# Performance work log

Hardware: AMD Instinct MI355X
Metric: run time of the kernel (lower is better)

## Reference

```python
import jax, jax.numpy as jnp
import numpy as np

B, S, F, H, D = 32, 512, 32, 8, 300   # batch, seq, n_features, hidden_dim, n_dim_model
FH = min(D, F)                        # flattened GRN hidden = min(n_dim_model, n_features)


def _p(key, shape, scale=0.05):
    return (jax.random.normal(key, shape) * scale).astype(jnp.float32)


def setup_inputs() -> dict:
    key = jax.random.key(0)
    ks = jax.random.split(key, 16)
    return {
        "x": jax.random.normal(ks[0], (B, S, F), dtype=jnp.float32),
        "pre_w": _p(ks[1], (F, H)), "pre_b": _p(ks[2], (F, H)),
        "sg_fc1_w": _p(ks[3], (F, H, H)), "sg_fc1_b": _p(ks[4], (F, H)),
        "sg_fc2_w": _p(ks[5], (F, H, D)), "sg_fc2_b": _p(ks[6], (F, D)),
        "sg_gate_w": _p(ks[7], (F, D, 2 * D)), "sg_gate_b": _p(ks[8], (F, 2 * D)),
        "sg_ln_g": jnp.ones((F, D), jnp.float32), "sg_ln_b": jnp.zeros((F, D), jnp.float32),
        "fl_fc1_w": _p(ks[9], (F * H, FH)), "fl_fc1_b": _p(ks[10], (FH,)),
        "fl_fc2_w": _p(ks[11], (FH, F)), "fl_fc2_b": _p(ks[12], (F,)),
        "fl_gate_w": _p(ks[13], (F, 2 * F)), "fl_gate_b": _p(ks[14], (2 * F,)),
        "fl_ln_g": jnp.ones((F,), jnp.float32), "fl_ln_b": jnp.zeros((F,), jnp.float32),
    }


def _interp_last(x, out_dim):
    # torch F.interpolate(mode='linear', align_corners=True) along the last axis
    in_dim = x.shape[-1]
    pos = jnp.arange(out_dim) * ((in_dim - 1) / (out_dim - 1))
    lo = jnp.floor(pos).astype(jnp.int32)
    hi = jnp.minimum(lo + 1, in_dim - 1)
    w = (pos - lo.astype(pos.dtype)).astype(x.dtype)
    return x[..., lo] * (1 - w) + x[..., hi] * w


def _layer_norm(x, g, b, eps=1e-5):
    m = jnp.mean(x, axis=-1, keepdims=True)
    v = jnp.var(x, axis=-1, keepdims=True)
    return (x - m) * jax.lax.rsqrt(v + eps) * g + b


def _forward(x, pre_w, pre_b, sg_fc1_w, sg_fc1_b, sg_fc2_w, sg_fc2_b,
             sg_gate_w, sg_gate_b, sg_ln_g, sg_ln_b,
             fl_fc1_w, fl_fc1_b, fl_fc2_w, fl_fc2_b, fl_gate_w, fl_gate_b,
             fl_ln_g, fl_ln_b):
    # per-feature prescaler: Linear(1, H) for each of F features, batched
    pre = x[..., None] * pre_w + pre_b                                   # [B,S,F,H]

    # per-feature GRN (H -> H -> D), batched over the feature axis f
    h = jax.nn.elu(jnp.einsum('bsfh,fhk->bsfk', pre, sg_fc1_w) + sg_fc1_b)
    h = jnp.einsum('bsfk,fkd->bsfd', h, sg_fc2_w) + sg_fc2_b             # [B,S,F,D]
    g = jnp.einsum('bsfd,fdp->bsfp', h, sg_gate_w) + sg_gate_b           # [B,S,F,2D]
    glu = g[..., :D] * jax.nn.sigmoid(g[..., D:])
    residual = _interp_last(pre, D)                                      # H -> D interpolate projection
    outputs = _layer_norm(glu + residual, sg_ln_g, sg_ln_b)              # [B,S,F,D]

    # flattened GRN on concatenated prescaler outputs (F*H -> FH -> F)
    flat = pre.reshape(pre.shape[0], pre.shape[1], F * H)                # matches torch.cat order
    fh = jax.nn.elu(flat @ fl_fc1_w + fl_fc1_b)
    fh = fh @ fl_fc2_w + fl_fc2_b                                        # [B,S,F]
    fg = fh @ fl_gate_w + fl_gate_b                                      # [B,S,2F]
    fglu = fg[..., :F] * jax.nn.sigmoid(fg[..., F:])
    wlogits = _layer_norm(fglu + _interp_last(flat, F), fl_ln_g, fl_ln_b)
    w = jax.nn.softmax(wlogits, axis=-1)                                 # [B,S,F]

    out = jnp.einsum('bsfd,bsf->bsd', outputs, w)                        # softmax-weighted sum over features
    return out, w[..., None, :]                                          # weights unsqueezed at dim -2


def reference(x, pre_w, pre_b, sg_fc1_w, sg_fc1_b, sg_fc2_w, sg_fc2_b,
              sg_gate_w, sg_gate_b, sg_ln_g, sg_ln_b,
              fl_fc1_w, fl_fc1_b, fl_fc2_w, fl_fc2_b, fl_gate_w, fl_gate_b,
              fl_ln_g, fl_ln_b):
    return _forward(x, pre_w, pre_b, sg_fc1_w, sg_fc1_b, sg_fc2_w, sg_fc2_b,
                    sg_gate_w, sg_gate_b, sg_ln_g, sg_ln_b,
                    fl_fc1_w, fl_fc1_b, fl_fc2_w, fl_fc2_b, fl_gate_w, fl_gate_b,
                    fl_ln_g, fl_ln_b)
```

## Files before the change

kernel.cpp:

```cpp
#include <hip/hip_runtime.h>
#include <hip/hip_bf16.h>

#define NB 32
#define NS 512
#define NF 32
#define NH 8
#define ND 300
#define NTOK (NB*NS)
#define TPW 8
#define WPB 4
#define TPB (TPW*WPB)

using bf16 = __hip_bfloat16;
typedef float v2f __attribute__((ext_vector_type(2)));

__device__ __forceinline__ float rcpf_(float x){ return __builtin_amdgcn_rcpf(x); }
__device__ __forceinline__ float rsqf_(float x){ return __builtin_amdgcn_rsqf(x); }
__device__ __forceinline__ float sigm(float x){ return rcpf_(1.0f + __expf(-x)); }
__device__ __forceinline__ float eluf(float x){ return x > 0.0f ? x : __expf(x) - 1.0f; }

__device__ __forceinline__ v2f fma2(v2f a, v2f b, v2f c){
    return __builtin_elementwise_fma(a, b, c);
}
__device__ __forceinline__ v2f fma2s(float s, v2f b, v2f c){
    return __builtin_elementwise_fma((v2f){s, s}, b, c);
}

template<int BF16>
__device__ __forceinline__ float ldf(const void* p, size_t i){
    if (BF16) return __bfloat162float(((const bf16*)p)[i]);
    return ((const float*)p)[i];
}
template<int BF16>
__device__ __forceinline__ void stf(void* p, size_t i, float v){
    if (BF16) ((bf16*)p)[i] = __float2bfloat16(v);
    else      ((float*)p)[i] = v;
}

__device__ __forceinline__ bool is_bf16(const void* ones){
    return *(const unsigned*)ones == 0x3F803F80u;
}

__device__ __forceinline__ v2f unpk(unsigned u){
    return (v2f){ __int_as_float((int)(u << 16)),
                  __int_as_float((int)(u & 0xFFFF0000u)) };
}
__device__ __forceinline__ unsigned pack_bf(float a, float b){
    bf16 ha = __float2bfloat16(a), hb = __float2bfloat16(b);
    return (unsigned)*(unsigned short*)&ha | ((unsigned)*(unsigned short*)&hb << 16);
}

template<int CTRL>
__device__ __forceinline__ float dppadd(float v){
    return v + __int_as_float(__builtin_amdgcn_update_dpp(
        0, __float_as_int(v), CTRL, 0xF, 0xF, true));
}
template<int CTRL>
__device__ __forceinline__ float dppmax(float v){
    return fmaxf(v, __int_as_float(__builtin_amdgcn_update_dpp(
        __float_as_int(v), __float_as_int(v), CTRL, 0xF, 0xF, false)));
}
__device__ __forceinline__ float rlane(float v, int l){
    return __int_as_float(__builtin_amdgcn_readlane(__float_as_int(v), l));
}
__device__ __forceinline__ float wsum64(float v){
    v = dppadd<0x111>(v); v = dppadd<0x112>(v); v = dppadd<0x114>(v); v = dppadd<0x118>(v);
    v = dppadd<0x142>(v); v = dppadd<0x143>(v);
    return rlane(v, 63);
}
__device__ __forceinline__ float rsum32(float v){
    v = dppadd<0x111>(v); v = dppadd<0x112>(v); v = dppadd<0x114>(v); v = dppadd<0x118>(v);
    return rlane(v, 15) + rlane(v, 31);
}
__device__ __forceinline__ float rmax32(float v){
    v = dppmax<0x111>(v); v = dppmax<0x112>(v); v = dppmax<0x114>(v); v = dppmax<0x118>(v);
    return fmaxf(rlane(v, 15), rlane(v, 31));
}

template<int BF16>
__device__ void precompute_body(const void* __restrict__ W2, const void* __restrict__ b2,
                                const void* __restrict__ Wg, const void* __restrict__ bg,
                                const void* __restrict__ sg_g, const void* __restrict__ sg_b,
                                unsigned* __restrict__ Crow,
                                float (*part)[64][18], float (*w2s)[2400], float (*b2s)[300])
{
    const int tid = threadIdx.x;
    const int l = tid & 63;
    const int q = tid >> 6;
    const int fd = blockIdx.x * 64 + l;
    const int f = fd / 300;
    const int d = fd % 300;

    const int fLo = (blockIdx.x * 64) / 300;
    const int fHi = (blockIdx.x * 64 + 63) / 300;

    for (int ff = 0; ff <= fHi - fLo; ++ff) {
        for (int idx = tid; idx < 2400; idx += 256)
            w2s[ff][idx] = ldf<BF16>(W2, (size_t)(fLo + ff) * 2400 + idx);
        for (int idx = tid; idx < 300; idx += 256)
            b2s[ff][idx] = ldf<BF16>(b2, (size_t)(fLo + ff) * 300 + idx);
    }
    __syncthreads();

    const float* myW2 = w2s[f - fLo];
    const float* myB2 = b2s[f - fLo];
    const size_t WgA = (size_t)f * 180000 + d;

    float accA[8] = {0,0,0,0,0,0,0,0};
    float accB[8] = {0,0,0,0,0,0,0,0};
    float bA = 0.f, bB = 0.f;
    for (int m = q * 75; m < q * 75 + 75; ++m) {
        float wa = ldf<BF16>(Wg, WgA + (size_t)m * 600);
        float wb = ldf<BF16>(Wg, WgA + (size_t)m * 600 + 300);
        #pragma unroll
        for (int k = 0; k < 8; ++k) {
            float w2v = myW2[k * 300 + m];
            accA[k] += w2v * wa;
            accB[k] += w2v * wb;
        }
        bA += myB2[m] * wa;
        bB += myB2[m] * wb;
    }
    #pragma unroll
    for (int k = 0; k < 8; ++k) { part[q][l][k] = accA[k]; part[q][l][8 + k] = accB[k]; }
    part[q][l][16] = bA;
    part[q][l][17] = bB;
    __syncthreads();

    unsigned* row = Crow + (size_t)fd * 12;
    for (int v = q; v < 12; v += 4) {
        if (v < 8) {
            float sA = part[0][l][v] + part[1][l][v] + part[2][l][v] + part[3][l][v];
            float sB = part[0][l][8+v] + part[1][l][8+v] + part[2][l][8+v] + part[3][l][8+v];
            row[v] = pack_bf(sA, sB);
        } else if (v == 8) {
            float s = part[0][l][16] + part[1][l][16] + part[2][l][16] + part[3][l][16];
            float bc = s + ldf<BF16>(bg, (size_t)f * 600 + d);
            row[8] = __float_as_uint(bc);
        } else if (v == 9) {
            float s = part[0][l][17] + part[1][l][17] + part[2][l][17] + part[3][l][17];
            float bc = s + ldf<BF16>(bg, (size_t)f * 600 + d + 300);
            row[9] = __float_as_uint(bc);
        } else if (v == 10) {
            row[10] = __float_as_uint(ldf<BF16>(sg_g, (size_t)f * 300 + d));
        } else {
            row[11] = __float_as_uint(ldf<BF16>(sg_b, (size_t)f * 300 + d));
        }
    }
}

__global__ void precompute_kernel(const void* __restrict__ W2, const void* __restrict__ b2,
                                  const void* __restrict__ Wg, const void* __restrict__ bg,
                                  const void* __restrict__ sg_g, const void* __restrict__ sg_b,
                                  unsigned* __restrict__ Crow)
{
    __shared__ float part[4][64][18];
    __shared__ float w2s[2][2400];
    __shared__ float b2s[2][300];
    if (is_bf16(sg_g))
        precompute_body<1>(W2, b2, Wg, bg, sg_g, sg_b, Crow, part, w2s, b2s);
    else
        precompute_body<0>(W2, b2, Wg, bg, sg_g, sg_b, Crow, part, w2s, b2s);
}

template<int BF16>
__device__ void vsn_body(const void* __restrict__ x,
                         const void* __restrict__ pre_w, const void* __restrict__ pre_b,
                         const void* __restrict__ W1,    const void* __restrict__ b1,
                         const void* __restrict__ fl1w,  const void* __restrict__ fl1b,
                         const void* __restrict__ fl2w,  const void* __restrict__ fl2b,
                         const void* __restrict__ flgw,  const void* __restrict__ flgb,
                         const void* __restrict__ flng,  const void* __restrict__ flnb,
                         const unsigned* __restrict__ Crow,
                         void* __restrict__ d_out, float* preS_, float* hS_)
{
    void* outMain = d_out;
    void* outW    = (char*)d_out + (size_t)NTOK * ND * (BF16 ? 2 : 4);

    const int tid  = threadIdx.x;
    const int wave = tid >> 6;
    const int lane = tid & 63;
    const int tokBase = blockIdx.x * TPB + wave * TPW;

    float* myPre = preS_ + wave * (TPW * 256);
    float* myH   = hS_   + wave * (TPW * 256);

    {
        float pw[4], pb[4];
        #pragma unroll
        for (int q = 0; q < 4; ++q) {
            pw[q] = ldf<BF16>(pre_w, 4 * lane + q);
            pb[q] = ldf<BF16>(pre_b, 4 * lane + q);
        }
        const int fidx = lane >> 1;
        #pragma unroll
        for (int t = 0; t < TPW; ++t) {
            float xv = ldf<BF16>(x, (size_t)(tokBase + t) * NF + fidx);
            float4 v;
            v.x = xv * pw[0] + pb[0];
            v.y = xv * pw[1] + pb[1];
            v.z = xv * pw[2] + pb[2];
            v.w = xv * pw[3] + pb[3];
            *(float4*)(&myPre[t * 256 + 4 * lane]) = v;
        }
    }

    {
        const int f  = lane >> 1;
        const int kh = (lane & 1) * 4;
        float w1r[8][4], b1r[4];
        #pragma unroll
        for (int m = 0; m < 8; ++m)
            #pragma unroll
            for (int q = 0; q < 4; ++q)
                w1r[m][q] = ldf<BF16>(W1, (size_t)(f * 8 + m) * 8 + kh + q);
        #pragma unroll
        for (int q = 0; q < 4; ++q) b1r[q] = ldf<BF16>(b1, f * 8 + kh + q);

        #pragma unroll
        for (int t = 0; t < TPW; ++t) {
            float pr[8];
            float4 pA = *(const float4*)(&myPre[t * 256 + f * 8]);
            float4 pB = *(const float4*)(&myPre[t * 256 + f * 8 + 4]);
            pr[0]=pA.x; pr[1]=pA.y; pr[2]=pA.z; pr[3]=pA.w;
            pr[4]=pB.x; pr[5]=pB.y; pr[6]=pB.z; pr[7]=pB.w;
            float a[4] = {b1r[0], b1r[1], b1r[2], b1r[3]};
            #pragma unroll
            for (int m = 0; m < 8; ++m)
                #pragma unroll
                for (int q = 0; q < 4; ++q)
                    a[q] += pr[m] * w1r[m][q];
            float4 hv4;
            hv4.x = eluf(a[0]); hv4.y = eluf(a[1]); hv4.z = eluf(a[2]); hv4.w = eluf(a[3]);
            *(float4*)(&myH[t * 256 + 4 * lane]) = hv4;
        }
    }

    const int jj = lane & 31;
    const int hB = lane >> 5;
    float wreg[TPW];
    {
        float f1b = (hB == 0) ? ldf<BF16>(fl1b, jj) : 0.0f;
        v2f p1v[4];
        #pragma unroll
        for (int g = 0; g < 4; ++g) p1v[g] = (v2f){f1b, f1b};
        for (int kg = 0; kg < 32; ++kg) {
            const int kk = hB * 128 + kg * 4;
            float4 pr[TPW];
            #pragma unroll
            for (int t = 0; t < TPW; ++t)
                pr[t] = *(const float4*)(&myPre[t * 256 + kk]);
            float w0 = ldf<BF16>(fl1w, (size_t)(kk + 0) * 32 + jj);
            float w1 = ldf<BF16>(fl1w, (size_t)(kk + 1) * 32 + jj);
            float w2 = ldf<BF16>(fl1w, (size_t)(kk + 2) * 32 + jj);
            float w3 = ldf<BF16>(fl1w, (size_t)(kk + 3) * 32 + jj);
            #pragma unroll
            for (int g = 0; g < 4; ++g) {
                p1v[g] = fma2((v2f){pr[2*g].x, pr[2*g+1].x}, (v2f){w0, w0}, p1v[g]);
                p1v[g] = fma2((v2f){pr[2*g].y, pr[2*g+1].y}, (v2f){w1, w1}, p1v[g]);
                p1v[g] = fma2((v2f){pr[2*g].z, pr[2*g+1].z}, (v2f){w2, w2}, p1v[g]);
                p1v[g] = fma2((v2f){pr[2*g].w, pr[2*g+1].w}, (v2f){w3, w3}, p1v[g]);
            }
        }
        float fhv[TPW];
        #pragma unroll
        for (int t = 0; t < TPW; ++t) {
            float p1 = (t & 1) ? p1v[t >> 1].y : p1v[t >> 1].x;
            fhv[t] = eluf(p1 + __shfl_xor(p1, 32));
        }

        float p2[TPW];
        float f2b = ldf<BF16>(fl2b, jj);
        #pragma unroll
        for (int t = 0; t < TPW; ++t) p2[t] = f2b;
        #pragma unroll
        for (int k = 0; k < 32; ++k) {
            float wv = ldf<BF16>(fl2w, k * 32 + jj);
            #pragma unroll
            for (int t = 0; t < TPW; ++t) p2[t] += rlane(fhv[t], k) * wv;
        }
        float p3[TPW];
        float fgbv = ldf<BF16>(flgb, lane);
        #pragma unroll
        for (int t = 0; t < TPW; ++t) p3[t] = fgbv;
        #pragma unroll
        for (int k = 0; k < 32; ++k) {
            float wv = ldf<BF16>(flgw, k * 64 + lane);
            #pragma unroll
            for (int t = 0; t < TPW; ++t) p3[t] += rlane(p2[t], k) * wv;
        }

        float lng = ldf<BF16>(flng, jj), lnb = ldf<BF16>(flnb, jj);
        float posB = (float)jj * (255.0f / 31.0f);
        int loB = (int)floorf(posB); loB = loB < 0 ? 0 : (loB > 254 ? 254 : loB);
        float frB = posB - (float)loB;

        #pragma unroll
        for (int t = 0; t < TPW; ++t) {
            float fgA  = __shfl(p3[t], jj);
            float fgB  = __shfl(p3[t], jj + 32);
            float fglu = fgA * sigm(fgB);
            float pl = myPre[t * 256 + loB];
            float ph = myPre[t * 256 + loB + 1];
            float tv = fglu + pl + frB * (ph - pl);
            float S1 = rsum32(tv);
            float S2 = rsum32(tv * tv);
            float mean = S1 * (1.0f / 32.0f);
            float var  = fmaxf(S2 * (1.0f / 32.0f) - mean * mean, 0.0f);
            float rs   = rsqf_(var + 1e-5f);
            float wl   = (tv - mean) * rs * lng + lnb;
            float mx   = rmax32(wl);
            float e    = __expf(wl - mx);
            float ss   = rsum32(e);
            float wv   = e * rcpf_(ss);
            wreg[t] = wv;
            if (lane < 32) stf<BF16>(outW, (size_t)(tokBase + t) * NF + lane, wv);
        }
    }

    int lo_[5]; float fr_[5];
    #pragma unroll
    for (int i = 0; i < 5; ++i) {
        int d = i * 64 + lane;
        float pos = (float)d * (7.0f / 299.0f);
        int lo = (int)floorf(pos); lo = lo < 0 ? 0 : (lo > 6 ? 6 : lo);
        lo_[i] = lo; fr_[i] = pos - (float)lo;
    }

    float acc[TPW][5];
    #pragma unroll
    for (int t = 0; t < TPW; ++t)
        #pragma unroll
        for (int i = 0; i < 5; ++i) acc[t][i] = 0.0f;

    for (int f = 0; f < NF; ++f) {
        v2f  P[5][8];
        float bcA[5], bcB[5], lgv[5], lbv[5];
        #pragma unroll
        for (int i = 0; i < 5; ++i) {
            int d = i * 64 + lane;
            bool ok = (d < ND);
            const uint4* row = (const uint4*)(Crow + ((size_t)f * ND + (ok ? d : ND - 1)) * 12);
            uint4 c0 = row[0], c1 = row[1], c2 = row[2];
            P[i][0] = unpk(c0.x); P[i][1] = unpk(c0.y);
            P[i][2] = unpk(c0.z); P[i][3] = unpk(c0.w);
            P[i][4] = unpk(c1.x); P[i][5] = unpk(c1.y);
            P[i][6] = unpk(c1.z); P[i][7] = unpk(c1.w);
            bcA[i] = __uint_as_float(c2.x);
            bcB[i] = __uint_as_float(c2.y);
            lgv[i] = __uint_as_float(c2.z);
            lbv[i] = __uint_as_float(c2.w);
        }

        #pragma unroll
        for (int t = 0; t < TPW; ++t) {
            float h[8];
            float4 h0 = *(const float4*)(&myH[t * 256 + f * 8]);
            float4 h1 = *(const float4*)(&myH[t * 256 + f * 8 + 4]);
            h[0]=h0.x; h[1]=h0.y; h[2]=h0.z; h[3]=h0.w;
            h[4]=h1.x; h[5]=h1.y; h[6]=h1.z; h[7]=h1.w;

            float tt[5], a1 = 0.f, a2 = 0.f;
            #pragma unroll
            for (int i = 0; i < 5; ++i) {
                int d = i * 64 + lane;
                bool ok = (d < ND);
                v2f g = {bcA[i], bcB[i]};
                g = fma2s(h[0], P[i][0], g);
                g = fma2s(h[1], P[i][1], g);
                g = fma2s(h[2], P[i][2], g);
                g = fma2s(h[3], P[i][3], g);
                g = fma2s(h[4], P[i][4], g);
                g = fma2s(h[5], P[i][5], g);
                g = fma2s(h[6], P[i][6], g);
                g = fma2s(h[7], P[i][7], g);
                int base = f * 8 + lo_[i];
                float pl = myPre[t * 256 + base];
                float ph = myPre[t * 256 + base + 1];
                float tv = g.x * sigm(g.y) + pl + fr_[i] * (ph - pl);
                tv = ok ? tv : 0.0f;
                tt[i] = tv; a1 += tv; a2 += tv * tv;
            }

            float S1 = wsum64(a1);
            float S2 = wsum64(a2);
            float mean = S1 * (1.0f / 300.0f);
            float var  = fmaxf(S2 * (1.0f / 300.0f) - mean * mean, 0.0f);
            float rs   = rsqf_(var + 1e-5f);
            float wf   = rlane(wreg[t], f);
            float wrs  = wf * rs;
            #pragma unroll
            for (int i = 0; i < 5; ++i) {
                int d = i * 64 + lane;
                if (d < ND) {
                    float a = wrs * lgv[i];
                    acc[t][i] += a * tt[i] + (wf * lbv[i] - a * mean);
                }
            }
        }
    }

    #pragma unroll
    for (int t = 0; t < TPW; ++t) {
        const size_t tok = (size_t)tokBase + t;
        #pragma unroll
        for (int i = 0; i < 5; ++i) {
            int d = i * 64 + lane;
            if (d < ND) stf<BF16>(outMain, tok * ND + d, acc[t][i]);
        }
    }
}

__launch_bounds__(256)
__global__ void vsn_main(const void* __restrict__ x,
                         const void* __restrict__ pre_w, const void* __restrict__ pre_b,
                         const void* __restrict__ W1,    const void* __restrict__ b1,
                         const void* __restrict__ fl1w,  const void* __restrict__ fl1b,
                         const void* __restrict__ fl2w,  const void* __restrict__ fl2b,
                         const void* __restrict__ flgw,  const void* __restrict__ flgb,
                         const void* __restrict__ flng,  const void* __restrict__ flnb,
                         const unsigned* __restrict__ Crow, void* __restrict__ d_out)
{
    __shared__ float preS_[WPB * TPW * 256];
    __shared__ float hS_[WPB * TPW * 256];
    if (is_bf16(flng))
        vsn_body<1>(x, pre_w, pre_b, W1, b1, fl1w, fl1b, fl2w, fl2b,
                    flgw, flgb, flng, flnb, Crow, d_out, preS_, hS_);
    else
        vsn_body<0>(x, pre_w, pre_b, W1, b1, fl1w, fl1b, fl2w, fl2b,
                    flgw, flgb, flng, flnb, Crow, d_out, preS_, hS_);
}

extern "C" void kernel_launch(void* const* d_in, const int* in_sizes, int n_in,
                              void* d_out, int out_size, void* d_ws, size_t ws_size,
                              hipStream_t stream)
{
    const void* x     = d_in[0];
    const void* pre_w = d_in[1];
    const void* pre_b = d_in[2];
    const void* W1    = d_in[3];
    const void* b1    = d_in[4];
    const void* W2    = d_in[5];
    const void* b2    = d_in[6];
    const void* Wg    = d_in[7];
    const void* bg    = d_in[8];
    const void* sg_g  = d_in[9];
    const void* sg_b  = d_in[10];
    const void* fl1w  = d_in[11];
    const void* fl1b  = d_in[12];
    const void* fl2w  = d_in[13];
    const void* fl2b  = d_in[14];
    const void* flgw  = d_in[15];
    const void* flgb  = d_in[16];
    const void* flng  = d_in[17];
    const void* flnb  = d_in[18];

    unsigned* Crow = (unsigned*)d_ws;

    precompute_kernel<<<150, 256, 0, stream>>>(W2, b2, Wg, bg, sg_g, sg_b, Crow);

    vsn_main<<<NTOK / TPB, 256, 0, stream>>>(x, pre_w, pre_b, W1, b1,
        fl1w, fl1b, fl2w, fl2b, flgw, flgb, flng, flnb, Crow, d_out);
}
```

Measured before the change: 322.6 us.

## Compute folded gate weights with bf16 MFMA per feature block

```diff
diff --git a/kernel.cpp b/kernel.cpp
--- a/kernel.cpp
+++ b/kernel.cpp
@@ -13,6 +13,8 @@
 
 using bf16 = __hip_bfloat16;
 typedef float v2f __attribute__((ext_vector_type(2)));
+typedef short s8v __attribute__((ext_vector_type(8)));
+typedef float f4v __attribute__((ext_vector_type(4)));
 
 __device__ __forceinline__ float rcpf_(float x){ return __builtin_amdgcn_rcpf(x); }
 __device__ __forceinline__ float rsqf_(float x){ return __builtin_amdgcn_rsqf(x); }
@@ -81,71 +83,74 @@
 __device__ void precompute_body(const void* __restrict__ W2, const void* __restrict__ b2,
                                 const void* __restrict__ Wg, const void* __restrict__ bg,
                                 const void* __restrict__ sg_g, const void* __restrict__ sg_b,
-                                unsigned* __restrict__ Crow,
-                                float (*part)[64][18], float (*w2s)[2400], float (*b2s)[300])
+                                unsigned* __restrict__ Crow, bf16* Als, char* buf)
 {
-    const int tid = threadIdx.x;
-    const int l = tid & 63;
-    const int q = tid >> 6;
-    const int fd = blockIdx.x * 64 + l;
-    const int f = fd / 300;
-    const int d = fd % 300;
-
-    const int fLo = (blockIdx.x * 64) / 300;
-    const int fHi = (blockIdx.x * 64 + 63) / 300;
-
-    for (int ff = 0; ff <= fHi - fLo; ++ff) {
-        for (int idx = tid; idx < 2400; idx += 256)
-            w2s[ff][idx] = ldf<BF16>(W2, (size_t)(fLo + ff) * 2400 + idx);
-        for (int idx = tid; idx < 300; idx += 256)
-            b2s[ff][idx] = ldf<BF16>(b2, (size_t)(fLo + ff) * 300 + idx);
-    }
+    const int tid  = threadIdx.x;
+    const int wave = tid >> 6;
+    const int lane = tid & 63;
+    const int f    = blockIdx.x;
+
+    bf16*  Bls = (bf16*)buf;
+    float* Ols = (float*)buf;
+
+    for (int idx = tid; idx < 16 * 328; idx += 256) {
+        int row = idx / 328, m = idx - row * 328;
+        float v = 0.f;
+        if (m < 300) {
+            if (row < 8)       v = ldf<BF16>(W2, (size_t)f * 2400 + row * 300 + m);
+            else if (row == 8) v = ldf<BF16>(b2, (size_t)f * 300 + m);
+        }
+        Als[row * 328 + m] = __float2bfloat16(v);
+    }
+
+    f4v acc[10];
+    #pragma unroll
+    for (int i = 0; i < 10; ++i) acc[i] = (f4v){0.f, 0.f, 0.f, 0.f};
+
+    const int arow = (lane & 15) * 328 + (lane >> 4) * 8;
+    const int bcol = (lane & 15);
+    const int bsub = (lane >> 4) * 8;
+
+    const int mmS = tid >> 3;
+    const int jbS = tid & 7;
+
+    for (int kk = 0; kk < 10; ++kk) {
+        const int m0 = kk * 32;
+        __syncthreads();
+        {
+            const int m = m0 + mmS;
+            const bool mok = (m < 300);
+            const size_t gb = (size_t)f * 180000 + (size_t)m * 600;
+            for (int j = jbS; j < 608; j += 8) {
+                float v = (mok && j < 600) ? ldf<BF16>(Wg, gb + j) : 0.f;
+                Bls[j * 40 + mmS] = __float2bfloat16(v);
+            }
+        }
+        __syncthreads();
+        for (int i = 0, tt = wave; tt < 38; tt += 4, ++i) {
+            s8v a = *(const s8v*)(Als + arow + m0);
+            s8v b = *(const s8v*)(Bls + (tt * 16 + bcol) * 40 + bsub);
+            acc[i] = __builtin_amdgcn_mfma_f32_16x16x32_bf16(a, b, acc[i], 0, 0, 0);
+        }
+    }
+
     __syncthreads();
-
-    const float* myW2 = w2s[f - fLo];
-    const float* myB2 = b2s[f - fLo];
-    const size_t WgA = (size_t)f * 180000 + d;
-
-    float accA[8] = {0,0,0,0,0,0,0,0};
-    float accB[8] = {0,0,0,0,0,0,0,0};
-    float bA = 0.f, bB = 0.f;
-    for (int m = q * 75; m < q * 75 + 75; ++m) {
-        float wa = ldf<BF16>(Wg, WgA + (size_t)m * 600);
-        float wb = ldf<BF16>(Wg, WgA + (size_t)m * 600 + 300);
-        #pragma unroll
-        for (int k = 0; k < 8; ++k) {
-            float w2v = myW2[k * 300 + m];
-            accA[k] += w2v * wa;
-            accB[k] += w2v * wb;
-        }
-        bA += myB2[m] * wa;
-        bB += myB2[m] * wb;
-    }
-    #pragma unroll
-    for (int k = 0; k < 8; ++k) { part[q][l][k] = accA[k]; part[q][l][8 + k] = accB[k]; }
-    part[q][l][16] = bA;
-    part[q][l][17] = bB;
+    for (int i = 0, tt = wave; tt < 38; tt += 4, ++i) {
+        #pragma unroll
+        for (int r = 0; r < 4; ++r)
+            Ols[((lane >> 4) * 4 + r) * 612 + tt * 16 + (lane & 15)] = acc[i][r];
+    }
     __syncthreads();
 
-    unsigned* row = Crow + (size_t)fd * 12;
-    for (int v = q; v < 12; v += 4) {
-        if (v < 8) {
-            float sA = part[0][l][v] + part[1][l][v] + part[2][l][v] + part[3][l][v];
-            float sB = part[0][l][8+v] + part[1][l][8+v] + part[2][l][8+v] + part[3][l][8+v];
-            row[v] = pack_bf(sA, sB);
-        } else if (v == 8) {
-            float s = part[0][l][16] + part[1][l][16] + part[2][l][16] + part[3][l][16];
-            float bc = s + ldf<BF16>(bg, (size_t)f * 600 + d);
-            row[8] = __float_as_uint(bc);
-        } else if (v == 9) {
-            float s = part[0][l][17] + part[1][l][17] + part[2][l][17] + part[3][l][17];
-            float bc = s + ldf<BF16>(bg, (size_t)f * 600 + d + 300);
-            row[9] = __float_as_uint(bc);
-        } else if (v == 10) {
-            row[10] = __float_as_uint(ldf<BF16>(sg_g, (size_t)f * 300 + d));
-        } else {
-            row[11] = __float_as_uint(ldf<BF16>(sg_b, (size_t)f * 300 + d));
-        }
+    for (int d = tid; d < 300; d += 256) {
+        unsigned* row = Crow + ((size_t)f * 300 + d) * 12;
+        #pragma unroll
+        for (int k = 0; k < 8; ++k)
+            row[k] = pack_bf(Ols[k * 612 + d], Ols[k * 612 + d + 300]);
+        row[8]  = __float_as_uint(Ols[8 * 612 + d]       + ldf<BF16>(bg, (size_t)f * 600 + d));
+        row[9]  = __float_as_uint(Ols[8 * 612 + d + 300] + ldf<BF16>(bg, (size_t)f * 600 + d + 300));
+        row[10] = __float_as_uint(ldf<BF16>(sg_g, (size_t)f * 300 + d));
+        row[11] = __float_as_uint(ldf<BF16>(sg_b, (size_t)f * 300 + d));
     }
 }
 
@@ -154,13 +159,12 @@
                                   const void* __restrict__ sg_g, const void* __restrict__ sg_b,
                                   unsigned* __restrict__ Crow)
 {
-    __shared__ float part[4][64][18];
-    __shared__ float w2s[2][2400];
-    __shared__ float b2s[2][300];
+    __shared__ __align__(16) bf16 Als[16 * 328];
+    __shared__ __align__(16) char buf[608 * 40 * 2];
     if (is_bf16(sg_g))
-        precompute_body<1>(W2, b2, Wg, bg, sg_g, sg_b, Crow, part, w2s, b2s);
+        precompute_body<1>(W2, b2, Wg, bg, sg_g, sg_b, Crow, Als, buf);
     else
-        precompute_body<0>(W2, b2, Wg, bg, sg_g, sg_b, Crow, part, w2s, b2s);
+        precompute_body<0>(W2, b2, Wg, bg, sg_g, sg_b, Crow, Als, buf);
 }
 
 template<int BF16>
@@ -457,7 +461,7 @@
 
     unsigned* Crow = (unsigned*)d_ws;
 
-    precompute_kernel<<<150, 256, 0, stream>>>(W2, b2, Wg, bg, sg_g, sg_b, Crow);
+    precompute_kernel<<<NF, 256, 0, stream>>>(W2, b2, Wg, bg, sg_g, sg_b, Crow);
 
     vsn_main<<<NTOK / TPB, 256, 0, stream>>>(x, pre_w, pre_b, W1, b1,
         fl1w, fl1b, fl2w, fl2b, flgw, flgb, flng, flnb, Crow, d_out);
```

Result: slower. 604.7 us (+87.5%).
